# Kernel optimization log

Hardware: AMD Instinct MI355X
Metric: run time of the kernel (lower is better)

Reference implementation:

```python
import jax, jax.numpy as jnp
import numpy as np

N = 65536      # active voxels
K = 27         # 3x3x3 SubM kernel taps
CIN = 4        # input voxel features (x,y,z,intensity)
C = 32         # stage-1 channels
NW = 2048      # number of attention windows
CAP = 32       # padded voxels per window (NW*CAP == N)
H = 2          # attention heads
HD = C // H    # head dim
R = 144        # quantized relative-position bins


def _subm_conv(feats, pairs, w):
    # spconv SubMConv3d as gather-scatter: pairs[k, i] = input voxel feeding
    # kernel tap k of output voxel i, or -1 if that neighbor is empty.
    valid = pairs >= 0                      # [K, N]
    idx = jnp.where(valid, pairs, 0)
    g = feats[idx] * valid[:, :, None].astype(feats.dtype)   # [K, N, Cin]
    return jnp.einsum('knc,kcd->nd', g, w)                    # [N, Cout]


def _bn_relu(x, g, b):
    # BatchNorm1d (eval, running stats folded) + ReLU
    return jax.nn.relu(x * g + b)


def _res_block(x, pairs, g1, b1, w1, g2, b2, w2):
    h = _bn_relu(x, g1, b1)
    h = _subm_conv(h, pairs, w1)
    h = _bn_relu(h, g2, b2)
    h = _subm_conv(h, pairs, w2)
    return x + h  # identity branch (in_ch == out_ch)


def _sphere_attention(x, win_idx, rel_idx, w_qkv, b_qkv, w_proj, b_proj, tq, tk, tv):
    xw = x[win_idx]                                           # [NW, CAP, C]
    qkv = (xw @ w_qkv + b_qkv).reshape(NW, CAP, 3, H, HD)
    q = qkv[:, :, 0] * (HD ** -0.5)
    k = qkv[:, :, 1]
    v = qkv[:, :, 2]
    scores = jnp.einsum('wihd,wjhd->whij', q, k)              # [NW, H, CAP, CAP]
    # quantized relative-position contributions (rel_query / rel_key)
    rq = tq[rel_idx]                                          # [NW, CAP, CAP, H, HD]
    rk = tk[rel_idx]
    scores = scores + jnp.einsum('wihd,wijhd->whij', q, rq)
    scores = scores + jnp.einsum('wjhd,wijhd->whij', k, rk)
    attn = jax.nn.softmax(scores, axis=-1)
    out = jnp.einsum('whij,wjhd->wihd', attn, v)
    out = out + jnp.einsum('whij,wijhd->wihd', attn, tv[rel_idx])  # rel_value
    out = out.reshape(NW, CAP, C) @ w_proj + b_proj
    # scatter windows back to the flat voxel list (win_idx is a permutation)
    y = jnp.zeros_like(x).at[win_idx.reshape(-1)].set(out.reshape(-1, C))
    return x + y  # residual (drop_path=0 in stage 1)


def setup_inputs() -> dict:
    key = jax.random.key(0)
    ks = jax.random.split(key, 16)
    feats = jax.random.normal(ks[0], (N, CIN), dtype=jnp.float32)
    pairs = jax.random.randint(ks[1], (K, N), 0, N, dtype=jnp.int32)
    drop = jax.random.uniform(ks[2], (K, N)) < 0.3
    pairs = jnp.where(drop, -1, pairs)
    pairs = pairs.at[K // 2].set(jnp.arange(N, dtype=jnp.int32))  # center tap = self
    win_idx = jax.random.permutation(ks[3], N).reshape(NW, CAP).astype(jnp.int32)
    rel_idx = jax.random.randint(ks[4], (NW, CAP, CAP), 0, R, dtype=jnp.int32)

    def w(k, shape, s=0.05):
        return jax.random.normal(k, shape, dtype=jnp.float32) * s

    wk = jax.random.split(ks[5], 12)
    inp = dict(feats=feats, pairs=pairs, win_idx=win_idx, rel_idx=rel_idx,
               w_in=w(wk[0], (K, CIN, C)),
               rb1_g1=jnp.ones((C,)), rb1_b1=jnp.zeros((C,)), rb1_w1=w(wk[1], (K, C, C)),
               rb1_g2=jnp.ones((C,)), rb1_b2=jnp.zeros((C,)), rb1_w2=w(wk[2], (K, C, C)),
               rb2_g1=jnp.ones((C,)), rb2_b1=jnp.zeros((C,)), rb2_w1=w(wk[3], (K, C, C)),
               rb2_g2=jnp.ones((C,)), rb2_b2=jnp.zeros((C,)), rb2_w2=w(wk[4], (K, C, C)),
               w_qkv=w(wk[5], (C, 3 * C), 0.1), b_qkv=jnp.zeros((3 * C,)),
               w_proj=w(wk[6], (C, C), 0.1), b_proj=jnp.zeros((C,)),
               tq=w(wk[7], (R, H, HD)), tk=w(wk[8], (R, H, HD)), tv=w(wk[9], (R, H, HD)))
    return inp


def reference(feats, pairs, win_idx, rel_idx, w_in,
              rb1_g1, rb1_b1, rb1_w1, rb1_g2, rb1_b2, rb1_w2,
              rb2_g1, rb2_b1, rb2_w1, rb2_g2, rb2_b2, rb2_w2,
              w_qkv, b_qkv, w_proj, b_proj, tq, tk, tv):
    x = _subm_conv(feats, pairs, w_in)                       # input_conv
    x = _res_block(x, pairs, rb1_g1, rb1_b1, rb1_w1, rb1_g2, rb1_b2, rb1_w2)
    x = _res_block(x, pairs, rb2_g1, rb2_b1, rb2_w1, rb2_g2, rb2_b2, rb2_w2)
    x = _sphere_attention(x, win_idx, rel_idx, w_qkv, b_qkv, w_proj, b_proj, tq, tk, tv)
    return x
```

## Files before the change

kernel.cpp:

```cpp
#include <hip/hip_runtime.h>

typedef unsigned short u16;
typedef unsigned int u32;

#define N_PTS 65536
#define KK 27
#define CIN 4
#define CC 32
#define NWIN 2048
#define CAP 32
#define NH 2
#define HD 16

typedef short s16x8 __attribute__((ext_vector_type(8)));
typedef float f32x4 __attribute__((ext_vector_type(4)));

__device__ __forceinline__ float bf2f(u16 h) { return __uint_as_float(((u32)h) << 16); }
__device__ __forceinline__ u16 f2bf(float f) {
    u32 u = __float_as_uint(f);
    u32 r = (u + 0x7FFFu + ((u >> 16) & 1u)) >> 16;
    return (u16)r;
}
__device__ __forceinline__ float ldany(const void* src, int i, bool isbf) {
    return isbf ? bf2f(((const u16*)src)[i]) : ((const float*)src)[i];
}
__device__ __forceinline__ u16 ldbf(const void* src, int i, bool isbf) {
    return isbf ? ((const u16*)src)[i] : f2bf(((const float*)src)[i]);
}

__global__ void detect_kernel(const u32* __restrict__ w, int* flag) {
    int t = threadIdx.x;
    int cnt = 0;
    for (int i = t; i < 4096; i += 256) {
        u32 e = (w[i] >> 7) & 0xFFu;
        cnt += (e >= 100 && e <= 140) ? 1 : 0;
    }
    __shared__ int red[256];
    red[t] = cnt;
    __syncthreads();
    for (int s = 128; s > 0; s >>= 1) {
        if (t < s) red[t] += red[t + s];
        __syncthreads();
    }
    if (t == 0) flag[0] = (red[0] > 2048) ? 1 : 0;
}

struct Ptrs { const void* p[24]; };

__global__ __launch_bounds__(256) void prep_all(
    Ptrs in, const int* __restrict__ flag,
    u16* __restrict__ fbf,
    u16* __restrict__ WpA1, u16* __restrict__ WpA2,
    u16* __restrict__ WpB1, u16* __restrict__ WpB2, u16* __restrict__ WpIN,
    u16* __restrict__ wqkvB, u16* __restrict__ wprojB,
    u16* __restrict__ tqB, u16* __restrict__ tkB, u16* __restrict__ tvb,
    float* __restrict__ Pf)
{
    bool isbf = flag[0] != 0;
    int seg = blockIdx.y;
    int i = blockIdx.x * 256 + threadIdx.x;
    if (seg == 0) {
        if (i < N_PTS * CIN) fbf[i] = ldbf(in.p[0], i, isbf);
        return;
    }
    if (seg <= 4) {
        if (i < 27648) {
            int e = i & 7, l = (i >> 3) & 63, dt = (i >> 9) & 1, k = i >> 10;
            const void* src = in.p[seg == 1 ? 7 : seg == 2 ? 10 : seg == 3 ? 13 : 16];
            u16* dst = seg == 1 ? WpA1 : seg == 2 ? WpA2 : seg == 3 ? WpB1 : WpB2;
            dst[i] = ldbf(src, k * 1024 + ((l >> 4) * 8 + e) * 32 + dt * 16 + (l & 15), isbf);
        }
        return;
    }
    if (seg == 5) {
        if (i < 4096) {
            int e = i & 7, l = (i >> 3) & 63, dt = (i >> 9) & 1, kk = i >> 10;
            int g = kk * 32 + (l >> 4) * 8 + e;
            int tp = g >> 2, c = g & 3;
            WpIN[i] = (tp < KK) ? ldbf(in.p[4], tp * 128 + c * 32 + dt * 16 + (l & 15), isbf) : (u16)0;
        }
        return;
    }
    if (seg == 6) {
        if (i < 3072) {
            int e = i & 7, l = (i >> 3) & 63, n = i >> 9;
            wqkvB[i] = ldbf(in.p[17], ((l >> 4) * 8 + e) * 96 + n * 16 + (l & 15), isbf);
        } else if (i < 4096) {
            int o2 = i - 3072;
            int e = o2 & 7, l = (o2 >> 3) & 63, n = o2 >> 9;
            wprojB[o2] = ldbf(in.p[19], ((l >> 4) * 8 + e) * 32 + n * 16 + (l & 15), isbf);
        }
        return;
    }
    if (seg == 7) {
        if (i < 9216) {
            int e = i & 7, l = (i >> 3) & 63, nn = i >> 9;
            int n = nn % 9, h = nn / 9, lr = l & 15, lg = l >> 4;
            int k = lg * 8 + e;
            tqB[i] = (k < HD) ? ldbf(in.p[21], (n * 16 + lr) * 32 + h * 16 + k, isbf) : (u16)0;
        } else if (i < 18432) {
            int o2 = i - 9216;
            int e = o2 & 7, l = (o2 >> 3) & 63, nn = o2 >> 9;
            int n = nn % 9, h = nn / 9, lr = l & 15, lg = l >> 4;
            int k = lg * 8 + e;
            tkB[o2] = (k < HD) ? ldbf(in.p[22], (n * 16 + lr) * 32 + h * 16 + k, isbf) : (u16)0;
        } else if (i < 23040) {
            int o2 = i - 18432;
            tvb[o2] = ldbf(in.p[23], o2, isbf);
        }
        return;
    }
    if (i < 256) {
        const int srcs[8] = {5, 6, 8, 9, 11, 12, 14, 15};
        Pf[i] = ldany(in.p[srcs[i >> 5]], i & 31, isbf);
    } else if (i < 352) {
        Pf[i] = ldany(in.p[18], i - 256, isbf);
    } else if (i < 384) {
        Pf[i] = ldany(in.p[20], i - 352, isbf);
    }
}

__global__ __launch_bounds__(256) void convin_mfma(
    const u16* __restrict__ fb, const int* __restrict__ pairs,
    const u16* __restrict__ Wp, const float* __restrict__ gb,
    float* __restrict__ xbuf, u16* __restrict__ act_out)
{
    int t = threadIdx.x;
    int wv = t >> 6, l = t & 63;
    int lr = l & 15, lg = l >> 4;
    int p0 = (blockIdx.x * 4 + wv) * 16;
    int rowaddr = p0 + lr;

    int ia[4], ib[4];
    u32 ma[4], mb[4];
#pragma unroll
    for (int kk = 0; kk < 4; kk++) {
        int t0 = kk * 8 + lg * 2;
        int ta = t0 < 26 ? t0 : 26;
        int tb = (t0 + 1) < 26 ? (t0 + 1) : 26;
        ia[kk] = pairs[ta * N_PTS + rowaddr];
        ib[kk] = pairs[tb * N_PTS + rowaddr];
        ma[kk] = (t0 < KK && ia[kk] >= 0) ? 0xFFFFFFFFu : 0u;
        mb[kk] = (t0 + 1 < KK && ib[kk] >= 0) ? 0xFFFFFFFFu : 0u;
    }
    uint2 qa[4], qb[4];
    s16x8 b0[4], b1[4];
#pragma unroll
    for (int kk = 0; kk < 4; kk++) {
        qa[kk] = *(const uint2*)(fb + (long)(ia[kk] < 0 ? 0 : ia[kk]) * CIN);
        qb[kk] = *(const uint2*)(fb + (long)(ib[kk] < 0 ? 0 : ib[kk]) * CIN);
        const s16x8* wb = (const s16x8*)Wp + kk * 128 + l;
        b0[kk] = wb[0];
        b1[kk] = wb[64];
    }

    f32x4 acc0 = {0.f, 0.f, 0.f, 0.f}, acc1 = {0.f, 0.f, 0.f, 0.f};
#pragma unroll
    for (int kk = 0; kk < 4; kk++) {
        union { uint4 q; s16x8 v; } a;
        a.q = make_uint4(qa[kk].x & ma[kk], qa[kk].y & ma[kk],
                         qb[kk].x & mb[kk], qb[kk].y & mb[kk]);
        acc0 = __builtin_amdgcn_mfma_f32_16x16x32_bf16(a.v, b0[kk], acc0, 0, 0, 0);
        acc1 = __builtin_amdgcn_mfma_f32_16x16x32_bf16(a.v, b1[kk], acc1, 0, 0, 0);
    }
    float g0 = gb[lr], b0v = gb[32 + lr], g1 = gb[16 + lr], b1v = gb[48 + lr];
#pragma unroll
    for (int r = 0; r < 4; r++) {
        int row = p0 + lg * 4 + r;
        long o0 = (long)row * 32 + lr, o1 = o0 + 16;
        float v0 = acc0[r], v1 = acc1[r];
        xbuf[o0] = v0; xbuf[o1] = v1;
        act_out[o0] = f2bf(fmaxf(fmaf(v0, g0, b0v), 0.f));
        act_out[o1] = f2bf(fmaxf(fmaf(v1, g1, b1v), 0.f));
    }
}

template <int M>
__global__ __launch_bounds__(256) void conv32_mfma(
    const u16* __restrict__ act_in, const int* __restrict__ pairs,
    const u16* __restrict__ Wp, const float* __restrict__ gb,
    float* __restrict__ xbuf, u16* __restrict__ act_out)
{
    int t = threadIdx.x;
    int wv = t >> 6, l = t & 63;
    int lr = l & 15, lg = l >> 4;
    int p0 = (blockIdx.x * 4 + wv) * 16;
    int rowaddr = p0 + lr;

    int idx[KK];
#pragma unroll
    for (int k = 0; k < KK; k++) idx[k] = pairs[k * N_PTS + rowaddr];

    uint4 qr[8];
    s16x8 b0r[8], b1r[8];
#pragma unroll
    for (int k = 0; k < 8; k++) {
        int ic = idx[k] < 0 ? 0 : idx[k];
        qr[k] = *(const uint4*)(act_in + (long)ic * CC + lg * 8);
        const s16x8* wb = (const s16x8*)Wp + k * 128 + l;
        b0r[k] = wb[0];
        b1r[k] = wb[64];
    }

    f32x4 acc0 = {0.f, 0.f, 0.f, 0.f}, acc1 = {0.f, 0.f, 0.f, 0.f};
#pragma unroll
    for (int k = 0; k < KK; k++) {
        int s = k & 7;
        uint4 q = qr[s];
        s16x8 w0 = b0r[s];
        s16x8 w1 = b1r[s];
        if (k + 8 < KK) {
            int kn = k + 8;
            int ic = idx[kn] < 0 ? 0 : idx[kn];
            qr[s] = *(const uint4*)(act_in + (long)ic * CC + lg * 8);
            const s16x8* wb = (const s16x8*)Wp + kn * 128 + l;
            b0r[s] = wb[0];
            b1r[s] = wb[64];
        }
        u32 msk = idx[k] >= 0 ? 0xFFFFFFFFu : 0u;
        q.x &= msk; q.y &= msk; q.z &= msk; q.w &= msk;
        union { uint4 q; s16x8 v; } a;
        a.q = q;
        acc0 = __builtin_amdgcn_mfma_f32_16x16x32_bf16(a.v, w0, acc0, 0, 0, 0);
        acc1 = __builtin_amdgcn_mfma_f32_16x16x32_bf16(a.v, w1, acc1, 0, 0, 0);
    }
    float g0 = 0.f, b0v = 0.f, g1 = 0.f, b1v = 0.f;
    if (M & 4) { g0 = gb[lr]; b0v = gb[32 + lr]; g1 = gb[16 + lr]; b1v = gb[48 + lr]; }
#pragma unroll
    for (int r = 0; r < 4; r++) {
        int row = p0 + lg * 4 + r;
        long o0 = (long)row * 32 + lr, o1 = o0 + 16;
        float v0 = acc0[r], v1 = acc1[r];
        if (M & 1) { v0 += xbuf[o0]; v1 += xbuf[o1]; }
        if (M & 2) { xbuf[o0] = v0; xbuf[o1] = v1; }
        if (M & 4) {
            act_out[o0] = f2bf(fmaxf(fmaf(v0, g0, b0v), 0.f));
            act_out[o1] = f2bf(fmaxf(fmaf(v1, g1, b1v), 0.f));
        }
    }
}

#define A5_RIDX 0
#define A5_QSB  4096
#define A5_KSB  6656
#define A5_VST  9216
#define A5_SC   11776
#define A5_BQ   20992
#define A5_BK   30208
#define A5_SIZE 39424

__global__ __launch_bounds__(256) void attn5_kernel(
    const float* __restrict__ x, const int* __restrict__ win_idx,
    const int* __restrict__ rel_idx,
    const u16* __restrict__ wqkvB, const u16* __restrict__ wprojB,
    const float* __restrict__ Pf,
    const u16* __restrict__ tqB, const u16* __restrict__ tkB, const u16* __restrict__ tvb,
    float* __restrict__ out)
{
    __shared__ __align__(16) char arena[A5_SIZE];
    int*   ridx = (int*)(arena + A5_RIDX);
    u16*   qsb  = (u16*)(arena + A5_QSB);
    u16*   ksb  = (u16*)(arena + A5_KSB);
    u16*   vsT  = (u16*)(arena + A5_VST);
    float* sc   = (float*)(arena + A5_SC);
    u16*   psb  = (u16*)(arena + A5_SC);
    u16*   Bq   = (u16*)(arena + A5_BQ);
    u16*   Bk   = (u16*)(arena + A5_BK);
    float* ot   = (float*)(arena + A5_BQ);

    int w = blockIdx.x, t = threadIdx.x;
    int wv = t >> 6, l = t & 63, lr = l & 15, lg = l >> 4;

    {
        int4 r4 = *(const int4*)(rel_idx + (long)w * 1024 + t * 4);
        *(int4*)(ridx + t * 4) = r4;
    }
    {
        const float* bqkv = Pf + 256;
        for (int pi = wv; pi < 12; pi += 4) {
            int n = pi >> 1, m = pi & 1;
            int gi = win_idx[w * 32 + m * 16 + lr];
            const float* xr = x + (long)gi * 32 + lg * 8;
            float4 x0 = *(const float4*)(xr);
            float4 x1 = *(const float4*)(xr + 4);
            union { s16x8 v; u16 h[8]; } a;
            a.h[0] = f2bf(x0.x); a.h[1] = f2bf(x0.y); a.h[2] = f2bf(x0.z); a.h[3] = f2bf(x0.w);
            a.h[4] = f2bf(x1.x); a.h[5] = f2bf(x1.y); a.h[6] = f2bf(x1.z); a.h[7] = f2bf(x1.w);
            s16x8 b = *(const s16x8*)(wqkvB + ((n * 64 + l) << 3));
            f32x4 acc = {0.f, 0.f, 0.f, 0.f};
            acc = __builtin_amdgcn_mfma_f32_16x16x32_bf16(a.v, b, acc, 0, 0, 0);
            int tt = n * 16 + lr;
            float bias = bqkv[tt];
#pragma unroll
            for (int r = 0; r < 4; r++) {
                int tok = m * 16 + lg * 4 + r;
                float v = acc[r] + bias;
                if (tt < 32)      qsb[tok * 40 + tt] = f2bf(v * 0.25f);
                else if (tt < 64) ksb[tok * 40 + (tt - 32)] = f2bf(v);
                else              vsT[(tt - 64) * 40 + tok] = f2bf(v);
            }
        }
    }
    __syncthreads();

    for (int h = 0; h < NH; h++) {
        for (int pi = wv; pi < 36; pi += 4) {
            int tb = pi >= 18 ? 1 : 0;
            int rem = pi - tb * 18;
            int m = rem / 9, n = rem % 9;
            const u16* src = tb ? ksb : qsb;
            const u16* tab = tb ? tkB : tqB;
            s16x8 a = {0, 0, 0, 0, 0, 0, 0, 0};
            if (lg < 2) a = *(const s16x8*)(src + (m * 16 + lr) * 40 + h * 16 + lg * 8);
            s16x8 b = *(const s16x8*)(tab + (((h * 9 + n) * 64 + l) << 3));
            f32x4 acc = {0.f, 0.f, 0.f, 0.f};
            acc = __builtin_amdgcn_mfma_f32_16x16x32_bf16(a, b, acc, 0, 0, 0);
            u16* dst = tb ? Bk : Bq;
#pragma unroll
            for (int r = 0; r < 4; r++)
                dst[(m * 16 + lg * 4 + r) * 144 + n * 16 + lr] = f2bf(acc[r]);
        }
        __syncthreads();
        for (int e = t; e < 1024; e += 256) {
            int i = e >> 5, j = e & 31, r = ridx[e];
            sc[h * 1152 + i * 36 + j] = bf2f(Bq[i * 144 + r]) + bf2f(Bk[j * 144 + r]);
        }
        __syncthreads();
    }

    for (int pi = wv; pi < 8; pi += 4) {
        int h = pi >> 2, m = (pi >> 1) & 1, n = pi & 1;
        s16x8 a = {0, 0, 0, 0, 0, 0, 0, 0}, b = {0, 0, 0, 0, 0, 0, 0, 0};
        if (lg < 2) {
            a = *(const s16x8*)(qsb + (m * 16 + lr) * 40 + h * 16 + lg * 8);
            b = *(const s16x8*)(ksb + (n * 16 + lr) * 40 + h * 16 + lg * 8);
        }
        f32x4 acc = {0.f, 0.f, 0.f, 0.f};
        acc = __builtin_amdgcn_mfma_f32_16x16x32_bf16(a, b, acc, 0, 0, 0);
#pragma unroll
        for (int r = 0; r < 4; r++)
            sc[h * 1152 + (m * 16 + lg * 4 + r) * 36 + n * 16 + lr] += acc[r];
    }
    __syncthreads();

    {
        int rr = t >> 2, sub = t & 3;
        int h = rr >> 5, i = rr & 31, j0 = sub * 8;
        const float* srow = sc + h * 1152 + i * 36 + j0;
        float pv[8];
        float m_ = -1e30f;
#pragma unroll
        for (int jj = 0; jj < 8; jj++) { pv[jj] = srow[jj]; m_ = fmaxf(m_, pv[jj]); }
        m_ = fmaxf(m_, __shfl_xor(m_, 1));
        m_ = fmaxf(m_, __shfl_xor(m_, 2));
        float sum = 0.f;
#pragma unroll
        for (int jj = 0; jj < 8; jj++) { pv[jj] = __expf(pv[jj] - m_); sum += pv[jj]; }
        sum += __shfl_xor(sum, 1);
        sum += __shfl_xor(sum, 2);
        float inv = 1.f / sum;
        __syncthreads();
        u16* prow = psb + h * 1280 + i * 40 + j0;
#pragma unroll
        for (int jj = 0; jj < 8; jj++) prow[jj] = f2bf(pv[jj] * inv);
    }
    __syncthreads();

    for (int o = t; o < CAP * 16; o += 256) {
        int i = o >> 4, hp = o & 15, h = hp >> 3;
        const u16* prow = psb + h * 1280 + i * 40;
        const int* rrow = ridx + i * 32;
        float a0 = 0.f, a1 = 0.f;
#pragma unroll 8
        for (int j = 0; j < CAP; j++) {
            int r = rrow[j];
            float p = bf2f(prow[j]);
            u32 tv2 = *(const u32*)(tvb + r * 32 + hp * 2);
            a0 = fmaf(p, __uint_as_float(tv2 << 16), a0);
            a1 = fmaf(p, __uint_as_float(tv2 & 0xffff0000u), a1);
        }
        ot[i * 36 + hp * 2] = a0;
        ot[i * 36 + hp * 2 + 1] = a1;
    }
    __syncthreads();

    {
        int h = wv >> 1, m = wv & 1;
        s16x8 a = *(const s16x8*)(psb + h * 1280 + (m * 16 + lr) * 40 + lg * 8);
        s16x8 b = *(const s16x8*)(vsT + (h * 16 + lr) * 40 + lg * 8);
        f32x4 acc = {0.f, 0.f, 0.f, 0.f};
        acc = __builtin_amdgcn_mfma_f32_16x16x32_bf16(a, b, acc, 0, 0, 0);
#pragma unroll
        for (int r = 0; r < 4; r++)
            ot[(m * 16 + lg * 4 + r) * 36 + h * 16 + lr] += acc[r];
    }
    __syncthreads();

    {
        int m = wv >> 1, n = wv & 1;
        union { s16x8 v; u16 h[8]; } a;
        const float* orow = ot + (m * 16 + lr) * 36 + lg * 8;
#pragma unroll
        for (int e = 0; e < 8; e++) a.h[e] = f2bf(orow[e]);
        s16x8 b = *(const s16x8*)(wprojB + ((n * 64 + l) << 3));
        f32x4 acc = {0.f, 0.f, 0.f, 0.f};
        acc = __builtin_amdgcn_mfma_f32_16x16x32_bf16(a.v, b, acc, 0, 0, 0);
        int c = n * 16 + lr;
        float bb = Pf[352 + c];
#pragma unroll
        for (int r = 0; r < 4; r++) {
            int tok = m * 16 + lg * 4 + r;
            int gi = win_idx[w * 32 + tok];
            out[(long)gi * 32 + c] = x[(long)gi * 32 + c] + bb + acc[r];
        }
    }
}

#define B_PF     0
#define B_FLAG   1536
#define B_ACTA   2048
#define B_ACTB   4196352
#define B_FEATS  8390656
#define B_WA1    8914944
#define B_WA2    8970240
#define B_WB1    9025536
#define B_WB2    9080832
#define B_WIN    9136128
#define B_WQKVB  9144320
#define B_WPROJB 9150464
#define B_TQBF   9152512
#define B_TKBF   9170944
#define B_TVBF   9189376

extern "C" void kernel_launch(void* const* d_in, const int* in_sizes, int n_in,
                              void* d_out, int out_size, void* d_ws, size_t ws_size,
                              hipStream_t stream) {
    const void* feats  = d_in[0];
    const int* pairs   = (const int*)d_in[1];
    const int* win_idx = (const int*)d_in[2];
    const int* rel_idx = (const int*)d_in[3];

    char* wsb = (char*)d_ws;
    float* Pf = (float*)(wsb + B_PF);
    int* flag = (int*)(wsb + B_FLAG);
    u16* actA = (u16*)(wsb + B_ACTA);
    u16* actB = (u16*)(wsb + B_ACTB);
    u16* fbf  = (u16*)(wsb + B_FEATS);
    u16* WpA1 = (u16*)(wsb + B_WA1);
    u16* WpA2 = (u16*)(wsb + B_WA2);
    u16* WpB1 = (u16*)(wsb + B_WB1);
    u16* WpB2 = (u16*)(wsb + B_WB2);
    u16* WpIN = (u16*)(wsb + B_WIN);
    u16* wqkvB  = (u16*)(wsb + B_WQKVB);
    u16* wprojB = (u16*)(wsb + B_WPROJB);
    u16* tqB = (u16*)(wsb + B_TQBF);
    u16* tkB = (u16*)(wsb + B_TKBF);
    u16* tvb = (u16*)(wsb + B_TVBF);
    float* X  = (float*)d_out;

    detect_kernel<<<1, 256, 0, stream>>>((const u32*)feats, flag);

    Ptrs pp;
    for (int i = 0; i < 24; i++) pp.p[i] = d_in[i];
    prep_all<<<dim3(1024, 9), 256, 0, stream>>>(pp, flag, fbf,
                                                WpA1, WpA2, WpB1, WpB2, WpIN,
                                                wqkvB, wprojB, tqB, tkB, tvb, Pf);

    convin_mfma<<<1024, 256, 0, stream>>>(fbf, pairs, WpIN, Pf + 0, X, actA);
    conv32_mfma<4><<<1024, 256, 0, stream>>>(actA, pairs, WpA1, Pf + 64,  X, actB);
    conv32_mfma<7><<<1024, 256, 0, stream>>>(actB, pairs, WpA2, Pf + 128, X, actA);
    conv32_mfma<4><<<1024, 256, 0, stream>>>(actA, pairs, WpB1, Pf + 192, X, actB);
    conv32_mfma<3><<<1024, 256, 0, stream>>>(actB, pairs, WpB2, Pf, X, actA);

    attn5_kernel<<<NWIN, 256, 0, stream>>>(X, win_idx, rel_idx,
                                           wqkvB, wprojB, Pf,
                                           tqB, tkB, tvb, X);
}
```

Baseline: 135.0 us.

## Stage conv32 weights in LDS and process two row tiles per wave

The 32-channel SubM conv kernels now copy all 27 taps of packed bf16 weights (about 54 KB) into shared memory once per block. MFMA B operands are then read from LDS instead of being prefetched from global memory per wave. Each wave handles two 16-row tiles, so the grid is halved to 512 blocks and the weight load is amortized over more output rows. In exchange, the large LDS footprint limits how many blocks fit per CU, the block-wide barrier adds a serial load phase, and there are fewer blocks to hide gather latency.

```diff
diff --git a/kernel.cpp b/kernel.cpp
--- a/kernel.cpp
+++ b/kernel.cpp
@@ -176,66 +176,77 @@
 }
 
 template <int M>
-__global__ __launch_bounds__(256) void conv32_mfma(
+__global__ __launch_bounds__(256) void conv32_lds(
     const u16* __restrict__ act_in, const int* __restrict__ pairs,
     const u16* __restrict__ Wp, const float* __restrict__ gb,
     float* __restrict__ xbuf, u16* __restrict__ act_out)
 {
+    __shared__ u16 wlds[KK * 1024];
     int t = threadIdx.x;
     int wv = t >> 6, l = t & 63;
     int lr = l & 15, lg = l >> 4;
-    int p0 = (blockIdx.x * 4 + wv) * 16;
-    int rowaddr = p0 + lr;
-
-    int idx[KK];
-#pragma unroll
-    for (int k = 0; k < KK; k++) idx[k] = pairs[k * N_PTS + rowaddr];
-
-    uint4 qr[8];
-    s16x8 b0r[8], b1r[8];
-#pragma unroll
-    for (int k = 0; k < 8; k++) {
-        int ic = idx[k] < 0 ? 0 : idx[k];
-        qr[k] = *(const uint4*)(act_in + (long)ic * CC + lg * 8);
-        const s16x8* wb = (const s16x8*)Wp + k * 128 + l;
-        b0r[k] = wb[0];
-        b1r[k] = wb[64];
-    }
-
-    f32x4 acc0 = {0.f, 0.f, 0.f, 0.f}, acc1 = {0.f, 0.f, 0.f, 0.f};
-#pragma unroll
-    for (int k = 0; k < KK; k++) {
-        int s = k & 7;
-        uint4 q = qr[s];
-        s16x8 w0 = b0r[s];
-        s16x8 w1 = b1r[s];
-        if (k + 8 < KK) {
-            int kn = k + 8;
-            int ic = idx[kn] < 0 ? 0 : idx[kn];
-            qr[s] = *(const uint4*)(act_in + (long)ic * CC + lg * 8);
-            const s16x8* wb = (const s16x8*)Wp + kn * 128 + l;
-            b0r[s] = wb[0];
-            b1r[s] = wb[64];
-        }
-        u32 msk = idx[k] >= 0 ? 0xFFFFFFFFu : 0u;
-        q.x &= msk; q.y &= msk; q.z &= msk; q.w &= msk;
-        union { uint4 q; s16x8 v; } a;
-        a.q = q;
-        acc0 = __builtin_amdgcn_mfma_f32_16x16x32_bf16(a.v, w0, acc0, 0, 0, 0);
-        acc1 = __builtin_amdgcn_mfma_f32_16x16x32_bf16(a.v, w1, acc1, 0, 0, 0);
-    }
+
+    {
+        const uint4* src = (const uint4*)Wp;
+        uint4* dst = (uint4*)wlds;
+#pragma unroll
+        for (int q = 0; q < 14; q++) {
+            int e = q * 256 + t;
+            if (e < 3456) dst[e] = src[e];
+        }
+    }
+    __syncthreads();
+
     float g0 = 0.f, b0v = 0.f, g1 = 0.f, b1v = 0.f;
     if (M & 4) { g0 = gb[lr]; b0v = gb[32 + lr]; g1 = gb[16 + lr]; b1v = gb[48 + lr]; }
-#pragma unroll
-    for (int r = 0; r < 4; r++) {
-        int row = p0 + lg * 4 + r;
-        long o0 = (long)row * 32 + lr, o1 = o0 + 16;
-        float v0 = acc0[r], v1 = acc1[r];
-        if (M & 1) { v0 += xbuf[o0]; v1 += xbuf[o1]; }
-        if (M & 2) { xbuf[o0] = v0; xbuf[o1] = v1; }
-        if (M & 4) {
-            act_out[o0] = f2bf(fmaxf(fmaf(v0, g0, b0v), 0.f));
-            act_out[o1] = f2bf(fmaxf(fmaf(v1, g1, b1v), 0.f));
+
+#pragma unroll
+    for (int tile = 0; tile < 2; tile++) {
+        int p0 = ((blockIdx.x * 4 + wv) * 2 + tile) * 16;
+        int rowaddr = p0 + lr;
+
+        int idx[KK];
+#pragma unroll
+        for (int k = 0; k < KK; k++) idx[k] = pairs[k * N_PTS + rowaddr];
+
+        uint4 qr[8];
+#pragma unroll
+        for (int k = 0; k < 8; k++) {
+            int ic = idx[k] < 0 ? 0 : idx[k];
+            qr[k] = *(const uint4*)(act_in + (long)ic * CC + lg * 8);
+        }
+
+        f32x4 acc0 = {0.f, 0.f, 0.f, 0.f}, acc1 = {0.f, 0.f, 0.f, 0.f};
+#pragma unroll
+        for (int k = 0; k < KK; k++) {
+            int s = k & 7;
+            uint4 q = qr[s];
+            if (k + 8 < KK) {
+                int kn = k + 8;
+                int ic = idx[kn] < 0 ? 0 : idx[kn];
+                qr[s] = *(const uint4*)(act_in + (long)ic * CC + lg * 8);
+            }
+            u32 msk = idx[k] >= 0 ? 0xFFFFFFFFu : 0u;
+            q.x &= msk; q.y &= msk; q.z &= msk; q.w &= msk;
+            union { uint4 q; s16x8 v; } a;
+            a.q = q;
+            const s16x8* wb = (const s16x8*)wlds + k * 128 + l;
+            s16x8 w0 = wb[0];
+            s16x8 w1 = wb[64];
+            acc0 = __builtin_amdgcn_mfma_f32_16x16x32_bf16(a.v, w0, acc0, 0, 0, 0);
+            acc1 = __builtin_amdgcn_mfma_f32_16x16x32_bf16(a.v, w1, acc1, 0, 0, 0);
+        }
+#pragma unroll
+        for (int r = 0; r < 4; r++) {
+            int row = p0 + lg * 4 + r;
+            long o0 = (long)row * 32 + lr, o1 = o0 + 16;
+            float v0 = acc0[r], v1 = acc1[r];
+            if (M & 1) { v0 += xbuf[o0]; v1 += xbuf[o1]; }
+            if (M & 2) { xbuf[o0] = v0; xbuf[o1] = v1; }
+            if (M & 4) {
+                act_out[o0] = f2bf(fmaxf(fmaf(v0, g0, b0v), 0.f));
+                act_out[o1] = f2bf(fmaxf(fmaf(v1, g1, b1v), 0.f));
+            }
         }
     }
 }
@@ -467,10 +478,10 @@
                                                 wqkvB, wprojB, tqB, tkB, tvb, Pf);
 
     convin_mfma<<<1024, 256, 0, stream>>>(fbf, pairs, WpIN, Pf + 0, X, actA);
-    conv32_mfma<4><<<1024, 256, 0, stream>>>(actA, pairs, WpA1, Pf + 64,  X, actB);
-    conv32_mfma<7><<<1024, 256, 0, stream>>>(actB, pairs, WpA2, Pf + 128, X, actA);
-    conv32_mfma<4><<<1024, 256, 0, stream>>>(actA, pairs, WpB1, Pf + 192, X, actB);
-    conv32_mfma<3><<<1024, 256, 0, stream>>>(actB, pairs, WpB2, Pf, X, actA);
+    conv32_lds<4><<<512, 256, 0, stream>>>(actA, pairs, WpA1, Pf + 64,  X, actB);
+    conv32_lds<7><<<512, 256, 0, stream>>>(actB, pairs, WpA2, Pf + 128, X, actA);
+    conv32_lds<4><<<512, 256, 0, stream>>>(actA, pairs, WpB1, Pf + 192, X, actB);
+    conv32_lds<3><<<512, 256, 0, stream>>>(actB, pairs, WpB2, Pf, X, actA);
 
     attn5_kernel<<<NWIN, 256, 0, stream>>>(X, win_idx, rel_idx,
                                            wqkvB, wprojB, Pf,
```

New measurement: 127.1 us. -5.8%, faster.
